# Kernel optimization log

Hardware: AMD Instinct MI355X
Metric: run time of the kernel (lower is better)

Reference implementation:

```python
import jax, jax.numpy as jnp
import numpy as np

N_SPEC = 256
M_IN = 16384
K_OUT = 4096


def _get_edges(wl):
    # bin edges at midpoints, extrapolated half a bin at each end
    mid = (wl[1:] + wl[:-1]) / 2
    first = wl[0] - (wl[1] - wl[0]) / 2
    last = wl[-1] + (wl[-1] - wl[-2]) / 2
    return jnp.concatenate([first[None], mid, last[None]])


def setup_inputs() -> dict:
    key = jax.random.key(0)
    k1, = jax.random.split(key, 1)
    # strictly increasing wavelength grids (nm); output grid coarser and inside input range
    wl_in = jnp.linspace(400.0, 900.0, M_IN, dtype=jnp.float32)
    wl_out = jnp.linspace(405.0, 895.0, K_OUT, dtype=jnp.float32)
    flux_in = jax.random.uniform(k1, (N_SPEC, M_IN), dtype=jnp.float32, minval=0.1, maxval=1.0)
    return {"wl_in": wl_in, "flux_in": flux_in, "wl_out": wl_out}


def reference(wl_in, flux_in, wl_out):
    # Flux-conserving rebinning (Spectrum.resample with method='conserve').
    edges_in = _get_edges(wl_in)    # (M+1,)
    edges_out = _get_edges(wl_out)  # (K+1,)
    delta_in = edges_in[1:] - edges_in[:-1]    # (M,)
    delta_out = edges_out[1:] - edges_out[:-1]  # (K,)
    # overlap length between each output bin k and input bin m -> (K, M)
    overlap_lo = jnp.maximum(edges_out[:-1, None], edges_in[None, :-1])
    overlap_hi = jnp.minimum(edges_out[1:, None], edges_in[None, 1:])
    overlap = jnp.clip(overlap_hi - overlap_lo, 0, None)
    frac = overlap / delta_in[None, :]  # fraction of input bin m landing in output bin k
    # sum_m flux[n,m] * frac[k,m] * delta_in[m]  (contraction instead of the (N,K,M) broadcast)
    w = frac * delta_in[None, :]  # (K, M)
    flux_out = jnp.einsum('nm,km->nk', flux_in, w) / delta_out[None, :]
    return flux_out
```

## Files before the change

### kernel.cpp

```cpp
#include <hip/hip_runtime.h>


#define NPB 2

__device__ __forceinline__ float edge_at(const float* __restrict__ wl, int n, int m) {
    if (m <= 0) return wl[0] - 0.5f * (wl[1] - wl[0]);
    if (m >= n) return wl[n - 1] + 0.5f * (wl[n - 1] - wl[n - 2]);
    return 0.5f * (wl[m - 1] + wl[m]);
}

__global__ __launch_bounds__(256) void rebin_v2_kernel(
    const float* __restrict__ wl_in, const float* __restrict__ flux_in,
    const float* __restrict__ wl_out, float* __restrict__ out,
    int M, int K, int N)
{
    int k = blockIdx.x * blockDim.x + threadIdx.x;
    if (k >= K) return;

    float eo_lo = edge_at(wl_out, K, k);
    float eo_hi = edge_at(wl_out, K, k + 1);
    float inv_d = 1.0f / (eo_hi - eo_lo);

    float w0 = wl_in[0];
    float e0 = w0 - 0.5f * (wl_in[1] - w0);
    float spacing = (wl_in[M - 1] - w0) / (float)(M - 1);
    int m0 = (int)floorf((eo_lo - e0) / spacing);
    m0 = max(0, min(M - 1, m0));
    while (m0 > 0 && edge_at(wl_in, M, m0) > eo_lo) --m0;
    while (m0 < M - 1 && edge_at(wl_in, M, m0 + 1) <= eo_lo) ++m0;

    int abase = m0 & ~3;

    float wa[8];
    float e_prev = edge_at(wl_in, M, abase);
    #pragma unroll
    for (int t = 0; t < 8; ++t) {
        float e_next = edge_at(wl_in, M, abase + t + 1);
        float ov = fminf(eo_hi, e_next) - fmaxf(eo_lo, e_prev);
        wa[t] = fmaxf(ov, 0.0f) * inv_d;
        e_prev = e_next;
    }

    int n0   = blockIdx.y * NPB;
    int nend = min(n0 + NPB, N);
    bool fast = (abase + 8 <= M);
    for (int n = n0; n < nend; ++n) {
        const float* fr = flux_in + (size_t)n * M;
        float acc;
        if (fast) {
            float4 f0 = *reinterpret_cast<const float4*>(fr + abase);
            float4 f1 = *reinterpret_cast<const float4*>(fr + abase + 4);
            acc = f0.x * wa[0];
            acc = fmaf(f0.y, wa[1], acc);
            acc = fmaf(f0.z, wa[2], acc);
            acc = fmaf(f0.w, wa[3], acc);
            acc = fmaf(f1.x, wa[4], acc);
            acc = fmaf(f1.y, wa[5], acc);
            acc = fmaf(f1.z, wa[6], acc);
            acc = fmaf(f1.w, wa[7], acc);
        } else {
            acc = 0.0f;
            #pragma unroll
            for (int t = 0; t < 8; ++t) {
                int idx = min(abase + t, M - 1);
                acc = fmaf(fr[idx], wa[t], acc);
            }
        }
        out[(size_t)n * K + k] = acc;
    }
}

extern "C" void kernel_launch(void* const* d_in, const int* in_sizes, int n_in,
                              void* d_out, int out_size, void* d_ws, size_t ws_size,
                              hipStream_t stream) {
    const float* wl_in   = (const float*)d_in[0];
    const float* flux_in = (const float*)d_in[1];
    const float* wl_out  = (const float*)d_in[2];
    float* out = (float*)d_out;

    int M = in_sizes[0];
    int K = in_sizes[2];
    int N = in_sizes[1] / M;

    dim3 block(256);
    dim3 grid((K + 255) / 256, (N + NPB - 1) / NPB);
    rebin_v2_kernel<<<grid, block, 0, stream>>>(wl_in, flux_in, wl_out, out, M, K, N);
}
```

Baseline: 73.34 us.

## Stage flux tile in LDS per block and process four spectra per block

```diff
diff --git a/kernel.cpp b/kernel.cpp
--- a/kernel.cpp
+++ b/kernel.cpp
@@ -1,7 +1,9 @@
 #include <hip/hip_runtime.h>
 
 
-#define NPB 2
+#define KT   256
+#define NPB  4
+#define LDSF 1536
 
 __device__ __forceinline__ float edge_at(const float* __restrict__ wl, int n, int m) {
     if (m <= 0) return wl[0] - 0.5f * (wl[1] - wl[0]);
@@ -9,47 +11,79 @@
     return 0.5f * (wl[m - 1] + wl[m]);
 }
 
-__global__ __launch_bounds__(256) void rebin_v2_kernel(
+__device__ __forceinline__ int find_m0(const float* __restrict__ wl_in, int M,
+                                       float eo_lo, float e0, float inv_sp) {
+    int m0 = (int)floorf((eo_lo - e0) * inv_sp);
+    m0 = max(0, min(M - 1, m0));
+    while (m0 > 0 && edge_at(wl_in, M, m0) > eo_lo) --m0;
+    while (m0 < M - 1 && edge_at(wl_in, M, m0 + 1) <= eo_lo) ++m0;
+    return m0;
+}
+
+__global__ __launch_bounds__(256) void rebin_v3_kernel(
     const float* __restrict__ wl_in, const float* __restrict__ flux_in,
     const float* __restrict__ wl_out, float* __restrict__ out,
     int M, int K, int N)
 {
-    int k = blockIdx.x * blockDim.x + threadIdx.x;
-    if (k >= K) return;
+    __shared__ float lds[NPB][LDSF];
 
-    float eo_lo = edge_at(wl_out, K, k);
-    float eo_hi = edge_at(wl_out, K, k + 1);
-    float inv_d = 1.0f / (eo_hi - eo_lo);
+    int k0 = blockIdx.x * KT;
+    int k  = k0 + threadIdx.x;
 
     float w0 = wl_in[0];
     float e0 = w0 - 0.5f * (wl_in[1] - w0);
     float spacing = (wl_in[M - 1] - w0) / (float)(M - 1);
-    int m0 = (int)floorf((eo_lo - e0) / spacing);
-    m0 = max(0, min(M - 1, m0));
-    while (m0 > 0 && edge_at(wl_in, M, m0) > eo_lo) --m0;
-    while (m0 < M - 1 && edge_at(wl_in, M, m0 + 1) <= eo_lo) ++m0;
+    float inv_sp = 1.0f / spacing;
 
-    int abase = m0 & ~3;
+    int kL = min(k0 + KT, K) - 1;
+    int m_start = find_m0(wl_in, M, edge_at(wl_out, K, k0), e0, inv_sp) & ~3;
+    int m_end   = (find_m0(wl_in, M, edge_at(wl_out, K, kL), e0, inv_sp) & ~3) + 8;
+    int cap = min(min(m_end - m_start, LDSF), M - m_start);
 
-    float wa[8];
-    float e_prev = edge_at(wl_in, M, abase);
-    #pragma unroll
-    for (int t = 0; t < 8; ++t) {
-        float e_next = edge_at(wl_in, M, abase + t + 1);
-        float ov = fminf(eo_hi, e_next) - fmaxf(eo_lo, e_prev);
-        wa[t] = fmaxf(ov, 0.0f) * inv_d;
-        e_prev = e_next;
+    int n0 = blockIdx.y * NPB;
+
+    int nq = cap >> 2;
+    for (int n = 0; n < NPB; ++n) {
+        if (n0 + n >= N) break;
+        const float4* src =
+            reinterpret_cast<const float4*>(flux_in + (size_t)(n0 + n) * M + m_start);
+        for (int q = threadIdx.x; q < nq; q += KT)
+            *reinterpret_cast<float4*>(&lds[n][q << 2]) = src[q];
     }
 
-    int n0   = blockIdx.y * NPB;
-    int nend = min(n0 + NPB, N);
-    bool fast = (abase + 8 <= M);
-    for (int n = n0; n < nend; ++n) {
-        const float* fr = flux_in + (size_t)n * M;
+    bool active = (k < K);
+    float wa[8];
+    int abase = m_start;
+    if (active) {
+        float eo_lo = edge_at(wl_out, K, k);
+        float eo_hi = edge_at(wl_out, K, k + 1);
+        float inv_d = 1.0f / (eo_hi - eo_lo);
+        int m0 = find_m0(wl_in, M, eo_lo, e0, inv_sp);
+        abase = m0 & ~3;
+        float e_prev = edge_at(wl_in, M, abase);
+        #pragma unroll
+        for (int t = 0; t < 8; ++t) {
+            float e_next = edge_at(wl_in, M, abase + t + 1);
+            wa[t] = fmaxf(fminf(eo_hi, e_next) - fmaxf(eo_lo, e_prev), 0.0f) * inv_d;
+            e_prev = e_next;
+        }
+    } else {
+        #pragma unroll
+        for (int t = 0; t < 8; ++t) wa[t] = 0.0f;
+    }
+
+    __syncthreads();
+
+    if (!active) return;
+
+    int off = abase - m_start;
+    bool fast = (off + 8 <= cap);
+    for (int n = 0; n < NPB; ++n) {
+        if (n0 + n >= N) break;
         float acc;
         if (fast) {
-            float4 f0 = *reinterpret_cast<const float4*>(fr + abase);
-            float4 f1 = *reinterpret_cast<const float4*>(fr + abase + 4);
+            float4 f0 = *reinterpret_cast<const float4*>(&lds[n][off]);
+            float4 f1 = *reinterpret_cast<const float4*>(&lds[n][off + 4]);
             acc = f0.x * wa[0];
             acc = fmaf(f0.y, wa[1], acc);
             acc = fmaf(f0.z, wa[2], acc);
@@ -59,14 +93,17 @@
             acc = fmaf(f1.z, wa[6], acc);
             acc = fmaf(f1.w, wa[7], acc);
         } else {
+            const float* fr = flux_in + (size_t)(n0 + n) * M;
             acc = 0.0f;
             #pragma unroll
             for (int t = 0; t < 8; ++t) {
-                int idx = min(abase + t, M - 1);
-                acc = fmaf(fr[idx], wa[t], acc);
+                int idx = abase + t;
+                int o = idx - m_start;
+                float fv = (o >= 0 && o < cap) ? lds[n][o] : fr[min(idx, M - 1)];
+                acc = fmaf(fv, wa[t], acc);
             }
         }
-        out[(size_t)n * K + k] = acc;
+        out[(size_t)(n0 + n) * K + k] = acc;
     }
 }
 
@@ -82,7 +119,7 @@
     int K = in_sizes[2];
     int N = in_sizes[1] / M;
 
-    dim3 block(256);
-    dim3 grid((K + 255) / 256, (N + NPB - 1) / NPB);
-    rebin_v2_kernel<<<grid, block, 0, stream>>>(wl_in, flux_in, wl_out, out, M, K, N);
+    dim3 block(KT);
+    dim3 grid((K + KT - 1) / KT, (N + NPB - 1) / NPB);
+    rebin_v3_kernel<<<grid, block, 0, stream>>>(wl_in, flux_in, wl_out, out, M, K, N);
 }
```

Result: no change. 74.06 us (+1.0%).
